# Kernel tuning notes

Measured on AMD Instinct MI355X. Metric: run time of the kernel, lower is better.

## Reference

```python
import jax, jax.numpy as jnp
import numpy as np

EMB = 1280
MD = 200
N = 20000
E = 200000
LN_EPS = 1e-5


def _layer_norm(x, g, b):
    mu = jnp.mean(x, axis=-1, keepdims=True)
    var = jnp.mean((x - mu) ** 2, axis=-1, keepdims=True)
    return (x - mu) * jax.lax.rsqrt(var + LN_EPS) * g + b


def _gat_conv(x, edge_index, edge_attr, W, We, a_src, a_dst, a_edge, bias, heads, C):
    """PyG GATConv (bias-free lin, edge_dim, add_self_loops with fill='mean')."""
    n = x.shape[0]
    src, dst = edge_index[0], edge_index[1]
    # self-loop edge_attr = mean of incoming edge_attr per dst node (0 if none)
    cnt = jax.ops.segment_sum(jnp.ones((edge_attr.shape[0],), x.dtype), dst, n)
    s = jax.ops.segment_sum(edge_attr, dst, n)
    loop_attr = jnp.where(cnt[:, None] > 0, s / jnp.maximum(cnt, 1.0)[:, None], 0.0)
    loop = jnp.arange(n)
    src = jnp.concatenate([src, loop])
    dst = jnp.concatenate([dst, loop])
    ea = jnp.concatenate([edge_attr, loop_attr], axis=0)
    h = (x @ W).reshape(n, heads, C)                      # [N,H,C]
    al_s = jnp.einsum('nhc,hc->nh', h, a_src)
    al_d = jnp.einsum('nhc,hc->nh', h, a_dst)
    eh = (ea @ We).reshape(-1, heads, C)                  # [E+N,H,C]
    al_e = jnp.einsum('ehc,hc->eh', eh, a_edge)
    alpha = jax.nn.leaky_relu(al_s[src] + al_d[dst] + al_e, 0.2)
    amax = jax.ops.segment_max(alpha, dst, n)
    amax = jnp.where(jnp.isfinite(amax), amax, 0.0)
    ex = jnp.exp(alpha - amax[dst])
    denom = jax.ops.segment_sum(ex, dst, n)
    w = ex / (denom[dst] + 1e-16)                         # segment softmax over dst
    out = jax.ops.segment_sum(h[src] * w[:, :, None], dst, n)
    return out.reshape(n, heads * C) + bias


def _forward(x, edge_index, edge_attr,
             ca_qw, ca_qb, ca_kw, ca_kb, ca_vw, ca_vb, ca_ow, ca_ob,
             g0_w, g0_ew, g0_as, g0_ad, g0_ae, g0_b, ln0_g, ln0_b,
             g1_w, g1_ew, g1_as, g1_ad, g1_ae, g1_b, ln1_g, ln1_b,
             g2_w, g2_ew, g2_as, g2_ad, g2_ae, g2_b, ln2_g, ln2_b,
             cls_w1, cls_b1, cls_w2, cls_b2):
    xe = x[:, :EMB]
    md = x[0, EMB:]
    # CrossAttention: single md vector -> K,V are [1,hidden]
    Q = xe @ ca_qw + ca_qb                                # [N,hid]
    K = md @ ca_kw + ca_kb                                # [hid]
    V = md @ ca_vw + ca_vb                                # [hid]
    scores = (Q @ K) / jnp.sqrt(jnp.asarray(Q.shape[-1], Q.dtype))  # [N]
    wts = jax.nn.softmax(scores, axis=0)[:, None]         # softmax over nodes
    attended = wts * V[None, :]                           # [N,hid]
    h = attended @ ca_ow + ca_ob + xe                     # [N,EMB]

    h = _gat_conv(h, edge_index, edge_attr, g0_w, g0_ew, g0_as, g0_ad, g0_ae, g0_b, 4, 256)
    h = jax.nn.relu(_layer_norm(h, ln0_g, ln0_b))
    h = _gat_conv(h, edge_index, edge_attr, g1_w, g1_ew, g1_as, g1_ad, g1_ae, g1_b, 4, 256)
    h = jax.nn.relu(_layer_norm(h, ln1_g, ln1_b))
    h = _gat_conv(h, edge_index, edge_attr, g2_w, g2_ew, g2_as, g2_ad, g2_ae, g2_b, 1, 256)
    h = jax.nn.relu(_layer_norm(h, ln2_g, ln2_b))

    g = jnp.mean(h, axis=0, keepdims=True)                # [1,256]
    g = jax.nn.relu(g @ cls_w1 + cls_b1)
    return g @ cls_w2 + cls_b2                            # [1,2]


def setup_inputs() -> dict:
    key = jax.random.key(0)
    ks = jax.random.split(key, 64)
    i = [0]
    def nrm(shape, scale=0.05):
        i[0] += 1
        return jax.random.normal(ks[i[0]], shape, jnp.float32) * scale
    inp = {}
    inp['x'] = nrm((N, EMB + MD), 1.0)
    inp['edge_index'] = jax.random.randint(ks[60], (2, E), 0, N, jnp.int64 if jax.config.read('jax_enable_x64') else jnp.int32)
    inp['edge_attr'] = jax.random.uniform(ks[61], (E, 1), jnp.float32)
    inp.update(ca_qw=nrm((EMB, 256)), ca_qb=jnp.zeros((256,), jnp.float32),
               ca_kw=nrm((MD, 256)), ca_kb=jnp.zeros((256,), jnp.float32),
               ca_vw=nrm((MD, 256)), ca_vb=jnp.zeros((256,), jnp.float32),
               ca_ow=nrm((256, EMB)), ca_ob=jnp.zeros((EMB,), jnp.float32))
    inp.update(g0_w=nrm((EMB, 1024)), g0_ew=nrm((1, 1024)), g0_as=nrm((4, 256)),
               g0_ad=nrm((4, 256)), g0_ae=nrm((4, 256)), g0_b=jnp.zeros((1024,), jnp.float32),
               ln0_g=jnp.ones((1024,), jnp.float32), ln0_b=jnp.zeros((1024,), jnp.float32))
    inp.update(g1_w=nrm((1024, 1024)), g1_ew=nrm((1, 1024)), g1_as=nrm((4, 256)),
               g1_ad=nrm((4, 256)), g1_ae=nrm((4, 256)), g1_b=jnp.zeros((1024,), jnp.float32),
               ln1_g=jnp.ones((1024,), jnp.float32), ln1_b=jnp.zeros((1024,), jnp.float32))
    inp.update(g2_w=nrm((1024, 256)), g2_ew=nrm((1, 256)), g2_as=nrm((1, 256)),
               g2_ad=nrm((1, 256)), g2_ae=nrm((1, 256)), g2_b=jnp.zeros((256,), jnp.float32),
               ln2_g=jnp.ones((256,), jnp.float32), ln2_b=jnp.zeros((256,), jnp.float32))
    inp.update(cls_w1=nrm((256, 128)), cls_b1=jnp.zeros((128,), jnp.float32),
               cls_w2=nrm((128, 2)), cls_b2=jnp.zeros((2,), jnp.float32))
    return inp


def reference(x, edge_index, edge_attr,
              ca_qw, ca_qb, ca_kw, ca_kb, ca_vw, ca_vb, ca_ow, ca_ob,
              g0_w, g0_ew, g0_as, g0_ad, g0_ae, g0_b, ln0_g, ln0_b,
              g1_w, g1_ew, g1_as, g1_ad, g1_ae, g1_b, ln1_g, ln1_b,
              g2_w, g2_ew, g2_as, g2_ad, g2_ae, g2_b, ln2_g, ln2_b,
              cls_w1, cls_b1, cls_w2, cls_b2):
    return _forward(x, edge_index, edge_attr,
                    ca_qw, ca_qb, ca_kw, ca_kb, ca_vw, ca_vb, ca_ow, ca_ob,
                    g0_w, g0_ew, g0_as, g0_ad, g0_ae, g0_b, ln0_g, ln0_b,
                    g1_w, g1_ew, g1_as, g1_ad, g1_ae, g1_b, ln1_g, ln1_b,
                    g2_w, g2_ew, g2_as, g2_ad, g2_ae, g2_b, ln2_g, ln2_b,
                    cls_w1, cls_b1, cls_w2, cls_b2)
```

## Files before the change

kernel.cpp:

```cpp
#include <hip/hip_runtime.h>
#include <hip/hip_bf16.h>
#include <math.h>

#define N_NODES 20000
#define N_EDGES 200000
#define XROW    1480

typedef __attribute__((ext_vector_type(8))) _Float16 f16x8;
typedef __attribute__((ext_vector_type(8))) unsigned short u16x8;
typedef __attribute__((ext_vector_type(4))) float f32x4v;

__device__ __forceinline__ float wsum(float v){
#pragma unroll
  for (int o=32;o>0;o>>=1) v += __shfl_down(v,o);
  return v;
}
__device__ __forceinline__ float wmax(float v){
#pragma unroll
  for (int o=32;o>0;o>>=1) v = fmaxf(v,__shfl_down(v,o));
  return v;
}
__device__ __forceinline__ float wsum_all(float v){
#pragma unroll
  for (int o=32;o>0;o>>=1) v += __shfl_xor(v,o);
  return v;
}
__device__ __forceinline__ float wmax_all(float v){
#pragma unroll
  for (int o=32;o>0;o>>=1) v = fmaxf(v,__shfl_xor(v,o));
  return v;
}

__device__ __forceinline__ unsigned short f2hu(float f){
  _Float16 h = (_Float16)f;
  return __builtin_bit_cast(unsigned short, h);
}
__device__ __forceinline__ float hu2f(unsigned short u){
  return (float)__builtin_bit_cast(_Float16, u);
}

__device__ __forceinline__ void async_copy16(void* lds, const void* g){
  __builtin_amdgcn_global_load_lds((const __attribute__((address_space(1))) void*)g,
                                   (__attribute__((address_space(3))) void*)lds, 16, 0, 0);
}

__global__ void edge_count_kernel(const int* __restrict__ ei, const float* __restrict__ ea,
                                  int* __restrict__ cnt, float* __restrict__ easum, int E){
  int e = blockIdx.x*256 + threadIdx.x;
  if (e >= E) return;
  int dst = ei[E + e];
  atomicAdd(&cnt[dst], 1);
  atomicAdd(&easum[dst], ea[e]);
}

__launch_bounds__(1024)
__global__ void scan_kernel(const int* __restrict__ cnt, const float* __restrict__ easum,
                            int* __restrict__ off, float* __restrict__ loop_attr, int n){
  __shared__ int buf[1024];
  const int PER = (N_NODES + 1023)/1024;
  int t = threadIdx.x;
  int base = t*PER;
  int local[PER];
  int s = 0;
#pragma unroll
  for (int k=0;k<PER;k++){
    int i = base + k;
    int v = (i<n)? cnt[i] : 0;
    local[k] = v;
    s += v;
  }
  buf[t] = s;
  __syncthreads();
  for (int d2=1; d2<1024; d2<<=1){
    int tv = (t>=d2)? buf[t-d2] : 0;
    __syncthreads();
    buf[t] += tv;
    __syncthreads();
  }
  int run = buf[t] - s;
#pragma unroll
  for (int k=0;k<PER;k++){
    int i = base + k;
    if (i < n){
      off[i] = run;
      int v = local[k];
      loop_attr[i] = (v>0) ? easum[i]/(float)v : 0.f;
      run += v;
    }
  }
  if (t == 1023) off[n] = buf[1023];
}

__global__ void edge_fill_kernel(const int* __restrict__ ei, const float* __restrict__ ea,
                                 const int* __restrict__ off, int* __restrict__ fill,
                                 int* __restrict__ csr_src, float* __restrict__ csr_ea, int E){
  int e = blockIdx.x*256 + threadIdx.x;
  if (e >= E) return;
  int dst = ei[E + e];
  int pos = off[dst] + atomicAdd(&fill[dst], 1);
  csr_src[pos] = ei[e];
  csr_ea[pos]  = ea[e];
}

__global__ void wt_f16_kernel(const float* __restrict__ W, int K, int N,
                              unsigned short* __restrict__ Wt){
  __shared__ float tile[32][33];
  int k0 = blockIdx.x*32, n0 = blockIdx.y*32;
  int tx = threadIdx.x & 31, ty = threadIdx.x >> 5;
  for (int r=ty; r<32; r+=8) tile[r][tx] = W[(size_t)(k0+r)*N + n0+tx];
  __syncthreads();
  for (int r=ty; r<32; r+=8){
    float w = tile[tx][r];
    Wt[(size_t)(n0+r)*K + k0+tx] = f2hu(w);
  }
}

__global__ void kv_kernel(const float* __restrict__ x,
                          const float* __restrict__ kw, const float* __restrict__ kb,
                          const float* __restrict__ vw, const float* __restrict__ vb,
                          float* __restrict__ Kv, float* __restrict__ Vv){
  int j = threadIdx.x;
  float ka = kb[j], va = vb[j];
  for (int k=0;k<200;k++){
    float m = x[1280+k];
    ka = fmaf(m, kw[k*256+j], ka);
    va = fmaf(m, vw[k*256+j], va);
  }
  Kv[j]=ka; Vv[j]=va;
}

__global__ void qkvo_kernel(const float* __restrict__ qw, const float* __restrict__ ow,
                            const float* __restrict__ Kv, const float* __restrict__ Vv,
                            float* __restrict__ qK, float* __restrict__ Vo){
  int b = blockIdx.x;
  if (b < 20){
    int wv = threadIdx.x>>6, lane = threadIdx.x&63;
    float4 k4 = ((const float4*)Kv)[lane];
    int w0 = b*4 + wv;
    for (int r = w0; r < 1280; r += 80){
      float4 q = *(const float4*)(qw + (size_t)r*256 + lane*4);
      float v = q.x*k4.x + q.y*k4.y + q.z*k4.z + q.w*k4.w;
      v = wsum(v);
      if (lane==0) qK[r] = v;
    }
  } else {
    int j = (b-20)*256 + threadIdx.x;
    float a=0;
    for (int i=0;i<256;i++) a = fmaf(Vv[i], ow[(size_t)i*1280+j], a);
    Vo[j]=a;
  }
}

__global__ void obw_kernel(const float* __restrict__ ob, const float* __restrict__ Vo,
                           const float* __restrict__ W, float* __restrict__ obW, float* __restrict__ VoW){
  int j = blockIdx.x*256 + threadIdx.x;
  int i0 = blockIdx.y*128;
  float a=0,b=0;
  for (int i=i0;i<i0+128;i++){
    float w = W[(size_t)i*1024+j];
    a = fmaf(ob[i], w, a);
    b = fmaf(Vo[i], w, b);
  }
  atomicAdd(&obW[j], a);
  atomicAdd(&VoW[j], b);
}

__launch_bounds__(256)
__global__ void xh_scores_kernel(const float* __restrict__ x, const float* __restrict__ qK,
                                 unsigned short* __restrict__ xh, float* __restrict__ scores, int n){
  __shared__ float qs[1280];
  int t = threadIdx.x;
  for (int i=t;i<1280;i+=256) qs[i]=qK[i];
  __syncthreads();
  int wid = t>>6, lane = t&63;
  int node = blockIdx.x*4 + wid;
  if (node >= n) return;
  const float* xr = x + (size_t)node*XROW;
  unsigned short* orow = xh + (size_t)node*1280;
  float acc = 0.f;
#pragma unroll
  for (int it=0; it<5; it++){
    int c4 = it*64 + lane;
    float4 v = *(const float4*)(xr + c4*4);
    ushort4 o;
    o.x = f2hu(v.x); o.y = f2hu(v.y); o.z = f2hu(v.z); o.w = f2hu(v.w);
    *(ushort4*)(orow + c4*4) = o;
    acc = fmaf(v.x, qs[c4*4+0], acc);
    acc = fmaf(v.y, qs[c4*4+1], acc);
    acc = fmaf(v.z, qs[c4*4+2], acc);
    acc = fmaf(v.w, qs[c4*4+3], acc);
  }
  acc = wsum(acc);
  if (lane==0) scores[node] = acc;
}

__launch_bounds__(1024)
__global__ void softmax_nodes(const float* __restrict__ scores, float* __restrict__ wts, int n){
  __shared__ float red[16];
  int t = threadIdx.x, lane=t&63, wid=t>>6;
  float m = -INFINITY;
  for (int i=t;i<n;i+=1024) m = fmaxf(m, scores[i]);
  m = wmax(m);
  if (lane==0) red[wid]=m;
  __syncthreads();
  if (t==0){ float r=red[0]; for (int k=1;k<16;k++) r=fmaxf(r,red[k]); red[0]=r; }
  __syncthreads();
  float M = red[0];
  __syncthreads();
  float z=0;
  for (int i=t;i<n;i+=1024) z += __expf((scores[i]-M)*(1.f/16.f));
  z = wsum(z);
  if (lane==0) red[wid]=z;
  __syncthreads();
  if (t==0){ float r=0; for (int k=0;k<16;k++) r+=red[k]; red[0]=r; }
  __syncthreads();
  float invZ = 1.f/red[0];
  for (int i=t;i<n;i+=1024) wts[i] = __expf((scores[i]-M)*(1.f/16.f))*invZ;
}

__launch_bounds__(256)
__global__ void gemm_f16(const unsigned short* __restrict__ A,
                         const unsigned short* __restrict__ B,
                         unsigned short* __restrict__ C, int M, int N, int K,
                         const float* __restrict__ addCol,
                         const float* __restrict__ vCol,
                         const float* __restrict__ wRow,
                         const float* __restrict__ a_src,
                         const float* __restrict__ a_dst,
                         float* __restrict__ alsp,
                         float* __restrict__ aldp)
{
  __shared__ short lds[2*2*128*32];

  const int ntc = N >> 7;
  const int sh  = __popc(ntc - 1);
  const int g   = blockIdx.y >> sh;
  const int nt  = blockIdx.y & (ntc - 1);
  const int band = blockIdx.x + (g << 3);
  if (band * 128 >= M) return;

  const int t = threadIdx.x;
  const int w = t>>6, l = t&63;
  const int bm = band*128, bn = nt*128;
  const int wr = (w>>1)*64, wc = (w&1)*64;
  const int half = w & 1;

  f32x4v acc[4][4];
#pragma unroll
  for (int i=0;i<4;i++)
#pragma unroll
    for (int j=0;j<4;j++) acc[i][j] = (f32x4v){0.f,0.f,0.f,0.f};

  const unsigned short* Ap[2]; const unsigned short* Bp[2];
  int ldsOff[2];
#pragma unroll
  for (int q=0;q<2;q++){
    int p    = (w*2+q)*64 + l;
    int sr   = p>>3, slot = p&7;
    int sl   = slot ^ (sr&7);
    int r    = sr*2 + (sl>>2);
    int kc   = (sl&3)*8;
    int rowA = bm + r; if (rowA > M-1) rowA = M-1;
    Ap[q] = A + (size_t)rowA*K + kc;
    Bp[q] = B + (size_t)(bn+r)*K + kc;
    ldsOff[q] = (w*2+q)*512;
  }

  const int nsteps = K >> 5;

#pragma unroll
  for (int q=0;q<2;q++) async_copy16(lds + ldsOff[q],        Ap[q]);
#pragma unroll
  for (int q=0;q<2;q++) async_copy16(lds + 4096 + ldsOff[q], Bp[q]);

  const int q4 = l>>4, m16 = l&15;

  for (int kt=0; kt<nsteps; ++kt){
    short* curb = lds + (kt&1)*8192;

    if (kt+1 < nsteps){
      short* nxt = lds + ((kt+1)&1)*8192;
      const int k0n = (kt+1)*32;
#pragma unroll
      for (int q=0;q<2;q++) async_copy16(nxt + ldsOff[q],        Ap[q] + k0n);
#pragma unroll
      for (int q=0;q<2;q++) async_copy16(nxt + 4096 + ldsOff[q], Bp[q] + k0n);
      asm volatile("s_waitcnt vmcnt(4)" ::: "memory");
    } else {
      asm volatile("s_waitcnt vmcnt(0)" ::: "memory");
    }
    __builtin_amdgcn_sched_barrier(0);
    __builtin_amdgcn_s_barrier();
    __builtin_amdgcn_sched_barrier(0);

    __builtin_amdgcn_s_setprio(1);
    {
      f16x8 af[4], bf[4];
#pragma unroll
      for (int i=0;i<4;i++){
        int ra = wr + i*16 + m16;
        af[i] = *(const f16x8*)&curb[(ra>>1)*64 + ((((((ra&1)<<2)+q4)) ^ ((ra>>1)&7))<<3)];
        int rb = wc + i*16 + m16;
        bf[i] = *(const f16x8*)&curb[4096 + (rb>>1)*64 + ((((((rb&1)<<2)+q4)) ^ ((rb>>1)&7))<<3)];
      }
#pragma unroll
      for (int i=0;i<4;i++)
#pragma unroll
        for (int j=0;j<4;j++)
          acc[i][j] = __builtin_amdgcn_mfma_f32_16x16x32_f16(af[i], bf[j], acc[i][j], 0,0,0);
    }
    __builtin_amdgcn_s_setprio(0);
    __builtin_amdgcn_sched_barrier(0);
    __builtin_amdgcn_s_barrier();
    __builtin_amdgcn_sched_barrier(0);
  }

  float* sred = (float*)lds;
  float* dred = sred + 256;
  float asv[4], adv[4];
#pragma unroll
  for (int j=0;j<4;j++){
    int n = bn + wc + j*16 + m16;
    asv[j] = a_src[n];
    adv[j] = a_dst[n];
  }
#pragma unroll
  for (int i=0;i<4;i++){
#pragma unroll
    for (int r=0;r<4;r++){
      int rloc = wr + i*16 + q4*4 + r;
      int m = bm + rloc;
      float wrow = addCol ? wRow[m < M ? m : M-1] : 0.f;
      float vj[4];
#pragma unroll
      for (int j=0;j<4;j++){
        int n = bn + wc + j*16 + m16;
        float v = acc[i][j][r];
        if (addCol) v += addCol[n] + wrow*vCol[n];
        vj[j] = v;
      }
      if (m < M){
        unsigned short* crow = C + (size_t)m*N;
#pragma unroll
        for (int j=0;j<4;j++) crow[bn + wc + j*16 + m16] = f2hu(vj[j]);
      }
      float s = vj[0]*asv[0] + vj[1]*asv[1] + vj[2]*asv[2] + vj[3]*asv[3];
      float d = vj[0]*adv[0] + vj[1]*adv[1] + vj[2]*adv[2] + vj[3]*adv[3];
#pragma unroll
      for (int o=1;o<16;o<<=1){ s += __shfl_xor(s,o); d += __shfl_xor(d,o); }
      if (m16 == 0){
        sred[half*128 + rloc] = s;
        dred[half*128 + rloc] = d;
      }
    }
  }
  __syncthreads();
  if (t < 128){
    int m = bm + t;
    if (m < M){
      alsp[(size_t)nt*M + m] = sred[t] + sred[128+t];
      aldp[(size_t)nt*M + m] = dred[t] + dred[128+t];
    }
  }
}

__global__ void als_combine(const float* __restrict__ alsp, const float* __restrict__ aldp,
                            float* __restrict__ als, float* __restrict__ ald, int M, int H,
                            const float* __restrict__ We, const float* __restrict__ a_edge,
                            float* __restrict__ we){
  if (blockIdx.x == 0){
    int wid = threadIdx.x>>6, lane = threadIdx.x&63;
    if (wid < H){
      const float4* w4 = (const float4*)(We + wid*256);
      const float4* a4 = (const float4*)(a_edge + wid*256);
      float4 a = w4[lane], b = a4[lane];
      float v = a.x*b.x + a.y*b.y + a.z*b.z + a.w*b.w;
      v = wsum(v);
      if (lane==0) we[wid]=v;
    }
  }
  int idx = blockIdx.x*256 + threadIdx.x;
  if (idx >= M*H) return;
  int m = idx / H, hh = idx - m*H;
  als[idx] = alsp[(size_t)(2*hh)*M + m] + alsp[(size_t)(2*hh+1)*M + m];
  ald[idx] = aldp[(size_t)(2*hh)*M + m] + aldp[(size_t)(2*hh+1)*M + m];
}

template<int H>
__launch_bounds__(256)
__global__ void gat_agg_ln_wave(const unsigned short* __restrict__ hmat,
                           const float* __restrict__ als, const float* __restrict__ ald,
                           const int* __restrict__ off, const int* __restrict__ csr_src,
                           const float* __restrict__ csr_ea, const float* __restrict__ loop_attr,
                           const float* __restrict__ we,
                           const float* __restrict__ bias,
                           const float* __restrict__ ln_g, const float* __restrict__ ln_b,
                           float* __restrict__ outf, unsigned short* __restrict__ outb, int n)
{
  constexpr int OUT = 256*H;
  constexpr int CPL = OUT/64;
  const int wv = threadIdx.x>>6, lane = threadIdx.x&63;
  const int i = blockIdx.x*4 + wv;
  __shared__ float wbuf_s[4][64*H];
  __shared__ int   sbuf_s[4][64];
  if (i >= n) return;
  float* wbuf = wbuf_s[wv];
  int*   sbuf = sbuf_s[wv];

  const int begin = off[i];
  const int deg   = off[i+1]-begin;
  const int S     = deg + 1;

  float aldi[H], wei[H];
#pragma unroll
  for (int hh=0;hh<H;hh++){ aldi[hh]=ald[(size_t)i*H+hh]; wei[hh]=we[hh]; }
  const float lea = loop_attr[i];

  const int head = (lane*CPL) >> 8;
  const int c0   = lane*CPL;
  float acc[CPL];
#pragma unroll
  for (int c=0;c<CPL;c++) acc[c]=0.f;

  if (S <= 64){
    int src = i; float ev = lea;
    if (lane < deg){ src = csr_src[begin+lane]; ev = csr_ea[begin+lane]; }
    const bool act = lane < S;
    sbuf[lane] = src;

    if constexpr (CPL==16){
      u16x8 a0r0,a0r1,a1r0,a1r1;
      {
        const unsigned short* r0p = hmat + (size_t)sbuf[0]*OUT + c0;
        a0r0 = *(const u16x8*)r0p; a0r1 = *(const u16x8*)(r0p+8);
        a1r0 = a0r0; a1r1 = a0r1;
        if (S > 1){
          const unsigned short* r1p = hmat + (size_t)sbuf[1]*OUT + c0;
          a1r0 = *(const u16x8*)r1p; a1r1 = *(const u16x8*)(r1p+8);
        }
      }
      float a[H];
#pragma unroll
      for (int hh=0;hh<H;hh++){
        float v = als[(size_t)src*H+hh] + aldi[hh] + ev*wei[hh];
        a[hh] = v>0.f ? v : 0.2f*v;
      }
#pragma unroll
      for (int hh=0;hh<H;hh++){
        float M = wmax_all(act ? a[hh] : -INFINITY);
        float e = act ? __expf(a[hh]-M) : 0.f;
        float Z = wsum_all(e);
        wbuf[lane*H+hh] = e / (Z + 1e-16f);
      }
      int j = 0;
      for (; j+2<S; j+=2){
        u16x8 n0r0,n0r1,n1r0,n1r1;
        {
          const unsigned short* rp = hmat + (size_t)sbuf[j+2]*OUT + c0;
          n0r0 = *(const u16x8*)rp; n0r1 = *(const u16x8*)(rp+8);
          n1r0 = n0r0; n1r1 = n0r1;
          if (j+3 < S){
            const unsigned short* rq = hmat + (size_t)sbuf[j+3]*OUT + c0;
            n1r0 = *(const u16x8*)rq; n1r1 = *(const u16x8*)(rq+8);
          }
        }
        float w0 = wbuf[j*H+head], w1 = wbuf[(j+1)*H+head];
#pragma unroll
        for (int c=0;c<8;c++){
          acc[c]   = fmaf(w0, hu2f(a0r0[c]), acc[c]);
          acc[8+c] = fmaf(w0, hu2f(a0r1[c]), acc[8+c]);
        }
#pragma unroll
        for (int c=0;c<8;c++){
          acc[c]   = fmaf(w1, hu2f(a1r0[c]), acc[c]);
          acc[8+c] = fmaf(w1, hu2f(a1r1[c]), acc[8+c]);
        }
        a0r0=n0r0; a0r1=n0r1; a1r0=n1r0; a1r1=n1r1;
      }
      {
        float w0 = wbuf[j*H+head];
#pragma unroll
        for (int c=0;c<8;c++){
          acc[c]   = fmaf(w0, hu2f(a0r0[c]), acc[c]);
          acc[8+c] = fmaf(w0, hu2f(a0r1[c]), acc[8+c]);
        }
        if (j+1 < S){
          float w1 = wbuf[(j+1)*H+head];
#pragma unroll
          for (int c=0;c<8;c++){
            acc[c]   = fmaf(w1, hu2f(a1r0[c]), acc[c]);
            acc[8+c] = fmaf(w1, hu2f(a1r1[c]), acc[8+c]);
          }
        }
      }
    } else {
      ushort4 a0, a1;
      {
        a0 = *(const ushort4*)(hmat + (size_t)sbuf[0]*OUT + c0);
        a1 = a0;
        if (S > 1) a1 = *(const ushort4*)(hmat + (size_t)sbuf[1]*OUT + c0);
      }
      float a[H];
#pragma unroll
      for (int hh=0;hh<H;hh++){
        float v = als[(size_t)src*H+hh] + aldi[hh] + ev*wei[hh];
        a[hh] = v>0.f ? v : 0.2f*v;
      }
#pragma unroll
      for (int hh=0;hh<H;hh++){
        float M = wmax_all(act ? a[hh] : -INFINITY);
        float e = act ? __expf(a[hh]-M) : 0.f;
        float Z = wsum_all(e);
        wbuf[lane*H+hh] = e / (Z + 1e-16f);
      }
      int j = 0;
      for (; j+2<S; j+=2){
        ushort4 n0, n1;
        n0 = *(const ushort4*)(hmat + (size_t)sbuf[j+2]*OUT + c0);
        n1 = n0;
        if (j+3 < S) n1 = *(const ushort4*)(hmat + (size_t)sbuf[j+3]*OUT + c0);
        float w0 = wbuf[j*H+head], w1 = wbuf[(j+1)*H+head];
        acc[0]=fmaf(w0,hu2f(a0.x),acc[0]); acc[1]=fmaf(w0,hu2f(a0.y),acc[1]);
        acc[2]=fmaf(w0,hu2f(a0.z),acc[2]); acc[3]=fmaf(w0,hu2f(a0.w),acc[3]);
        acc[0]=fmaf(w1,hu2f(a1.x),acc[0]); acc[1]=fmaf(w1,hu2f(a1.y),acc[1]);
        acc[2]=fmaf(w1,hu2f(a1.z),acc[2]); acc[3]=fmaf(w1,hu2f(a1.w),acc[3]);
        a0=n0; a1=n1;
      }
      {
        float w0 = wbuf[j*H+head];
        acc[0]=fmaf(w0,hu2f(a0.x),acc[0]); acc[1]=fmaf(w0,hu2f(a0.y),acc[1]);
        acc[2]=fmaf(w0,hu2f(a0.z),acc[2]); acc[3]=fmaf(w0,hu2f(a0.w),acc[3]);
        if (j+1 < S){
          float w1 = wbuf[(j+1)*H+head];
          acc[0]=fmaf(w1,hu2f(a1.x),acc[0]); acc[1]=fmaf(w1,hu2f(a1.y),acc[1]);
          acc[2]=fmaf(w1,hu2f(a1.z),acc[2]); acc[3]=fmaf(w1,hu2f(a1.w),acc[3]);
        }
      }
    }
  } else {
    float rm[H];
#pragma unroll
    for (int hh=0;hh<H;hh++) rm[hh] = -INFINITY;
    for (int s=lane; s<S; s+=64){
      int src = (s<deg)? csr_src[begin+s] : i;
      float ev = (s<deg)? csr_ea[begin+s] : lea;
#pragma unroll
      for (int hh=0;hh<H;hh++){
        float v = als[(size_t)src*H+hh] + aldi[hh] + ev*wei[hh];
        v = v>0.f? v : 0.2f*v;
        rm[hh] = fmaxf(rm[hh], v);
      }
    }
    float M[H], es[H];
#pragma unroll
    for (int hh=0;hh<H;hh++){ M[hh]=wmax_all(rm[hh]); es[hh]=0.f; }
    for (int s=lane; s<S; s+=64){
      int src = (s<deg)? csr_src[begin+s] : i;
      float ev = (s<deg)? csr_ea[begin+s] : lea;
#pragma unroll
      for (int hh=0;hh<H;hh++){
        float v = als[(size_t)src*H+hh] + aldi[hh] + ev*wei[hh];
        v = v>0.f? v : 0.2f*v;
        es[hh] += __expf(v - M[hh]);
      }
    }
    float invZ[H];
#pragma unroll
    for (int hh=0;hh<H;hh++) invZ[hh] = 1.f/(wsum_all(es[hh]) + 1e-16f);
    for (int cb=0; cb<S; cb+=64){
      int m = min(64, S-cb);
      int s = cb + lane;
      if (s < S){
        int src = (s<deg)? csr_src[begin+s] : i;
        float ev = (s<deg)? csr_ea[begin+s] : lea;
        sbuf[lane] = src;
#pragma unroll
        for (int hh=0;hh<H;hh++){
          float v = als[(size_t)src*H+hh] + aldi[hh] + ev*wei[hh];
          v = v>0.f? v : 0.2f*v;
          wbuf[lane*H+hh] = __expf(v - M[hh]) * invZ[hh];
        }
      }
      for (int j=0;j<m;j++){
        int sj = sbuf[j];
        float wj = wbuf[j*H+head];
        const unsigned short* row = hmat + (size_t)sj*OUT + c0;
        if constexpr (CPL==16){
          u16x8 r0 = *(const u16x8*)(row);
          u16x8 r1 = *(const u16x8*)(row+8);
#pragma unroll
          for (int c=0;c<8;c++){
            acc[c]   = fmaf(wj, hu2f(r0[c]), acc[c]);
            acc[8+c] = fmaf(wj, hu2f(r1[c]), acc[8+c]);
          }
        } else {
          ushort4 r = *(const ushort4*)(row);
          acc[0]=fmaf(wj,hu2f(r.x),acc[0]); acc[1]=fmaf(wj,hu2f(r.y),acc[1]);
          acc[2]=fmaf(wj,hu2f(r.z),acc[2]); acc[3]=fmaf(wj,hu2f(r.w),acc[3]);
        }
      }
    }
  }

  float vals[CPL];
  float ls=0.f;
#pragma unroll
  for (int c=0;c<CPL;c+=4){
    float4 b4 = *(const float4*)(bias + c0 + c);
    vals[c]=acc[c]+b4.x; vals[c+1]=acc[c+1]+b4.y; vals[c+2]=acc[c+2]+b4.z; vals[c+3]=acc[c+3]+b4.w;
    ls += vals[c]+vals[c+1]+vals[c+2]+vals[c+3];
  }
  float mu = wsum_all(ls) * (1.f/OUT);
  float lv=0.f;
#pragma unroll
  for (int c=0;c<CPL;c++){ float d=vals[c]-mu; lv += d*d; }
  float inv = rsqrtf(wsum_all(lv)*(1.f/OUT) + 1e-5f);

  if (outb){
    if constexpr (CPL==16){
#pragma unroll
      for (int c=0;c<CPL;c+=8){
        u16x8 o;
#pragma unroll
        for (int k=0;k<8;k++){
          float g = ln_g[c0+c+k], b = ln_b[c0+c+k];
          o[k] = f2hu(fmaxf((vals[c+k]-mu)*inv*g + b, 0.f));
        }
        *(u16x8*)(outb + (size_t)i*OUT + c0 + c) = o;
      }
    } else {
      ushort4 o;
      o.x = f2hu(fmaxf((vals[0]-mu)*inv*ln_g[c0+0] + ln_b[c0+0], 0.f));
      o.y = f2hu(fmaxf((vals[1]-mu)*inv*ln_g[c0+1] + ln_b[c0+1], 0.f));
      o.z = f2hu(fmaxf((vals[2]-mu)*inv*ln_g[c0+2] + ln_b[c0+2], 0.f));
      o.w = f2hu(fmaxf((vals[3]-mu)*inv*ln_g[c0+3] + ln_b[c0+3], 0.f));
      *(ushort4*)(outb + (size_t)i*OUT + c0) = o;
    }
  } else {
#pragma unroll
    for (int c=0;c<CPL;c+=4){
      float4 g4 = *(const float4*)(ln_g + c0 + c);
      float4 b4 = *(const float4*)(ln_b + c0 + c);
      float4 o;
      o.x = fmaxf((vals[c+0]-mu)*inv*g4.x + b4.x, 0.f);
      o.y = fmaxf((vals[c+1]-mu)*inv*g4.y + b4.y, 0.f);
      o.z = fmaxf((vals[c+2]-mu)*inv*g4.z + b4.z, 0.f);
      o.w = fmaxf((vals[c+3]-mu)*inv*g4.w + b4.w, 0.f);
      *(float4*)(outf + (size_t)i*OUT + c0 + c) = o;
    }
  }
}

__global__ void colsum_kernel(const float* __restrict__ h2, float* __restrict__ gsum, int n){
  int c = threadIdx.x;
  float acc=0;
  for (int i=blockIdx.x;i<n;i+=gridDim.x) acc += h2[(size_t)i*256 + c];
  atomicAdd(&gsum[c], acc);
}

__launch_bounds__(128)
__global__ void cls_kernel(const float* __restrict__ gsum,
                           const float* __restrict__ w1, const float* __restrict__ b1,
                           const float* __restrict__ w2, const float* __restrict__ b2,
                           float* __restrict__ outp){
  __shared__ float g[256];
  __shared__ float hid[128];
  int t = threadIdx.x;
  g[t]     = gsum[t]    *(1.f/N_NODES);
  g[t+128] = gsum[t+128]*(1.f/N_NODES);
  __syncthreads();
  float a = b1[t];
  for (int c=0;c<256;c++) a = fmaf(g[c], w1[c*128+t], a);
  hid[t] = fmaxf(a, 0.f);
  __syncthreads();
  if (t<2){
    float o = b2[t];
    for (int j=0;j<128;j++) o = fmaf(hid[j], w2[j*2+t], o);
    outp[t] = o;
  }
}

extern "C" void kernel_launch(void* const* d_in, const int* in_sizes, int n_in,
                              void* d_out, int out_size, void* d_ws, size_t ws_size,
                              hipStream_t stream)
{
  const float* x      = (const float*)d_in[0];
  const int*   ei     = (const int*)  d_in[1];
  const float* ea     = (const float*)d_in[2];
  const float* ca_qw  = (const float*)d_in[3];
  const float* ca_kw  = (const float*)d_in[5];
  const float* ca_kb  = (const float*)d_in[6];
  const float* ca_vw  = (const float*)d_in[7];
  const float* ca_vb  = (const float*)d_in[8];
  const float* ca_ow  = (const float*)d_in[9];
  const float* ca_ob  = (const float*)d_in[10];
  const float* g0_w   = (const float*)d_in[11];
  const float* g0_ew  = (const float*)d_in[12];
  const float* g0_as  = (const float*)d_in[13];
  const float* g0_ad  = (const float*)d_in[14];
  const float* g0_ae  = (const float*)d_in[15];
  const float* g0_b   = (const float*)d_in[16];
  const float* ln0_g  = (const float*)d_in[17];
  const float* ln0_b  = (const float*)d_in[18];
  const float* g1_w   = (const float*)d_in[19];
  const float* g1_ew  = (const float*)d_in[20];
  const float* g1_as  = (const float*)d_in[21];
  const float* g1_ad  = (const float*)d_in[22];
  const float* g1_ae  = (const float*)d_in[23];
  const float* g1_b   = (const float*)d_in[24];
  const float* ln1_g  = (const float*)d_in[25];
  const float* ln1_b  = (const float*)d_in[26];
  const float* g2_w   = (const float*)d_in[27];
  const float* g2_ew  = (const float*)d_in[28];
  const float* g2_as  = (const float*)d_in[29];
  const float* g2_ad  = (const float*)d_in[30];
  const float* g2_ae  = (const float*)d_in[31];
  const float* g2_b   = (const float*)d_in[32];
  const float* ln2_g  = (const float*)d_in[33];
  const float* ln2_b  = (const float*)d_in[34];
  const float* cls_w1 = (const float*)d_in[35];
  const float* cls_b1 = (const float*)d_in[36];
  const float* cls_w2 = (const float*)d_in[37];
  const float* cls_b2 = (const float*)d_in[38];
  float* outp = (float*)d_out;

  const int N = N_NODES, E = N_EDGES;

  char* base = (char*)d_ws;
  size_t o = 0;
  auto alloc = [&](size_t bytes)->void*{
    void* p = base + o;
    o += (bytes + 255) & ~(size_t)255;
    return p;
  };
  unsigned short* hF   = (unsigned short*)alloc((size_t)N*1024*2);
  unsigned short* Af   = (unsigned short*)alloc((size_t)N*1280*2);
  float*          h2   = (float*)         alloc((size_t)N*256*4);
  unsigned short* Wt   = (unsigned short*)alloc((size_t)1280*1024*2);
  float* alsp      = (float*)alloc((size_t)8*N*4);
  float* aldp      = (float*)alloc((size_t)8*N*4);
  float* als       = (float*)alloc((size_t)2*N*4*4);
  float* ald       = als + (size_t)N*4;
  float* scores    = (float*)alloc((size_t)N*4);
  float* wts       = (float*)alloc((size_t)N*4);
  int*   cnt       = (int*)  alloc((size_t)N*4);
  float* easum     = (float*)alloc((size_t)N*4);
  int*   off       = (int*)  alloc((size_t)(N+1)*4);
  int*   fill      = (int*)  alloc((size_t)N*4);
  int*   csr_src   = (int*)  alloc((size_t)E*4);
  float* csr_ea    = (float*)alloc((size_t)E*4);
  float* loop_attr = (float*)alloc((size_t)N*4);
  float* Kv        = (float*)alloc(256*4);
  float* Vv        = (float*)alloc(256*4);
  float* qK        = (float*)alloc(1280*4);
  float* Vo        = (float*)alloc(1280*4);
  float* obW       = (float*)alloc(1024*4);
  float* VoW       = (float*)alloc(1024*4);
  float* web       = (float*)alloc(16*4);
  float* gsum      = (float*)alloc(256*4);

  hipMemsetAsync(cnt,   0, (size_t)N*4, stream);
  hipMemsetAsync(easum, 0, (size_t)N*4, stream);
  hipMemsetAsync(fill,  0, (size_t)N*4, stream);
  hipMemsetAsync(gsum,  0, 256*4,       stream);
  hipMemsetAsync(obW,   0, 1024*4,      stream);
  hipMemsetAsync(VoW,   0, 1024*4,      stream);

  int eblocks = (E + 255)/256;
  edge_count_kernel<<<eblocks,256,0,stream>>>(ei, ea, cnt, easum, E);
  scan_kernel<<<1,1024,0,stream>>>(cnt, easum, off, loop_attr, N);
  edge_fill_kernel<<<eblocks,256,0,stream>>>(ei, ea, off, fill, csr_src, csr_ea, E);

  kv_kernel<<<1,256,0,stream>>>(x, ca_kw, ca_kb, ca_vw, ca_vb, Kv, Vv);
  qkvo_kernel<<<25,256,0,stream>>>(ca_qw, ca_ow, Kv, Vv, qK, Vo);
  xh_scores_kernel<<<(N+3)/4,256,0,stream>>>(x, qK, Af, scores, N);
  obw_kernel<<<dim3(4,10),256,0,stream>>>(ca_ob, Vo, g0_w, obW, VoW);
  softmax_nodes<<<1,1024,0,stream>>>(scores, wts, N);

  const int mTiles  = (N + 127)/128;
  const int mGroups = (mTiles + 7)/8;
  const int NB4 = (N + 3)/4;

  wt_f16_kernel<<<dim3(1280/32, 1024/32),256,0,stream>>>(g0_w, 1280, 1024, Wt);
  gemm_f16<<<dim3(8, mGroups*8),256,0,stream>>>(Af, Wt, hF, N, 1024, 1280, obW, VoW, wts,
                                                g0_as, g0_ad, alsp, aldp);
  als_combine<<<(N*4+255)/256,256,0,stream>>>(alsp, aldp, als, ald, N, 4, g0_ew, g0_ae, web);
  gat_agg_ln_wave<4><<<NB4,256,0,stream>>>(hF, als, ald, off, csr_src, csr_ea, loop_attr,
                                           web, g0_b, ln0_g, ln0_b, nullptr, Af, N);

  wt_f16_kernel<<<dim3(1024/32, 1024/32),256,0,stream>>>(g1_w, 1024, 1024, Wt);
  gemm_f16<<<dim3(8, mGroups*8),256,0,stream>>>(Af, Wt, hF, N, 1024, 1024, nullptr, nullptr, nullptr,
                                                g1_as, g1_ad, alsp, aldp);
  als_combine<<<(N*4+255)/256,256,0,stream>>>(alsp, aldp, als, ald, N, 4, g1_ew, g1_ae, web);
  gat_agg_ln_wave<4><<<NB4,256,0,stream>>>(hF, als, ald, off, csr_src, csr_ea, loop_attr,
                                           web, g1_b, ln1_g, ln1_b, nullptr, Af, N);

  wt_f16_kernel<<<dim3(1024/32, 256/32),256,0,stream>>>(g2_w, 1024, 256, Wt);
  gemm_f16<<<dim3(8, mGroups*2),256,0,stream>>>(Af, Wt, hF, N, 256, 1024, nullptr, nullptr, nullptr,
                                                g2_as, g2_ad, alsp, aldp);
  als_combine<<<(N+255)/256,256,0,stream>>>(alsp, aldp, als, ald, N, 1, g2_ew, g2_ae, web);
  gat_agg_ln_wave<1><<<NB4,256,0,stream>>>(hF, als, ald, off, csr_src, csr_ea, loop_attr,
                                           web, g2_b, ln2_g, ln2_b, h2, nullptr, N);

  colsum_kernel<<<256,256,0,stream>>>(h2, gsum, N);
  cls_kernel<<<1,128,0,stream>>>(gsum, cls_w1, cls_b1, cls_w2, cls_b2, outp);

  (void)in_sizes; (void)n_in; (void)out_size; (void)ws_size;
}
```

Measured before the change: 798.8 us.

## Parallelize node softmax and KV projection across blocks, fold normalization into GEMM

Replaces the single-block node softmax with multi-block max and sum-of-exp kernels that combine results through global atomics, using an order-preserving integer encoding for the float max. The per-row softmax weight is now computed inside the first GEMM epilogue from the raw score, the global max and the sum, so the weights array is no longer written. The K/V projection is split across 8 blocks with atomic accumulation. This removes serial single-block kernels from the critical path, at the cost of extra memsets, an extra launch, and nondeterministic float atomic summation.

```diff
diff --git a/kernel.cpp b/kernel.cpp
--- a/kernel.cpp
+++ b/kernel.cpp
@@ -37,6 +37,15 @@
 }
 __device__ __forceinline__ float hu2f(unsigned short u){
   return (float)__builtin_bit_cast(_Float16, u);
+}
+
+__device__ __forceinline__ unsigned fenc(float f){
+  unsigned b = __float_as_uint(f);
+  return (b & 0x80000000u) ? ~b : (b | 0x80000000u);
+}
+__device__ __forceinline__ float fdec(unsigned u){
+  unsigned b = (u & 0x80000000u) ? (u & 0x7FFFFFFFu) : ~u;
+  return __uint_as_float(b);
 }
 
 __device__ __forceinline__ void async_copy16(void* lds, const void* g){
@@ -120,13 +129,16 @@
                           const float* __restrict__ vw, const float* __restrict__ vb,
                           float* __restrict__ Kv, float* __restrict__ Vv){
   int j = threadIdx.x;
-  float ka = kb[j], va = vb[j];
-  for (int k=0;k<200;k++){
+  int k0 = blockIdx.x*25;
+  float ka = 0.f, va = 0.f;
+  if (blockIdx.x == 0){ ka = kb[j]; va = vb[j]; }
+  for (int k=k0;k<k0+25;k++){
     float m = x[1280+k];
     ka = fmaf(m, kw[k*256+j], ka);
     va = fmaf(m, vw[k*256+j], va);
   }
-  Kv[j]=ka; Vv[j]=va;
+  atomicAdd(&Kv[j], ka);
+  atomicAdd(&Vv[j], va);
 }
 
 __global__ void qkvo_kernel(const float* __restrict__ qw, const float* __restrict__ ow,
@@ -194,28 +206,32 @@
   if (lane==0) scores[node] = acc;
 }
 
-__launch_bounds__(1024)
-__global__ void softmax_nodes(const float* __restrict__ scores, float* __restrict__ wts, int n){
-  __shared__ float red[16];
-  int t = threadIdx.x, lane=t&63, wid=t>>6;
+__global__ void smax_kernel(const float* __restrict__ scores, unsigned* __restrict__ gmaxu, int n){
+  __shared__ float red[4];
+  int t = threadIdx.x, lane = t&63, wv = t>>6;
   float m = -INFINITY;
-  for (int i=t;i<n;i+=1024) m = fmaxf(m, scores[i]);
-  m = wmax(m);
-  if (lane==0) red[wid]=m;
+  for (int i = blockIdx.x*256 + t; i < n; i += gridDim.x*256) m = fmaxf(m, scores[i]);
+  m = wmax_all(m);
+  if (lane==0) red[wv] = m;
   __syncthreads();
-  if (t==0){ float r=red[0]; for (int k=1;k<16;k++) r=fmaxf(r,red[k]); red[0]=r; }
+  if (t==0){
+    float r = fmaxf(fmaxf(red[0],red[1]), fmaxf(red[2],red[3]));
+    atomicMax(gmaxu, fenc(r));
+  }
+}
+
+__global__ void zsum_kernel(const float* __restrict__ scores, const unsigned* __restrict__ gmaxu,
+                            float* __restrict__ gz, int n){
+  __shared__ float red[4];
+  float M = fdec(*gmaxu);
+  int t = threadIdx.x, lane = t&63, wv = t>>6;
+  float z = 0.f;
+  for (int i = blockIdx.x*256 + t; i < n; i += gridDim.x*256)
+    z += __expf((scores[i]-M)*(1.f/16.f));
+  z = wsum_all(z);
+  if (lane==0) red[wv] = z;
   __syncthreads();
-  float M = red[0];
-  __syncthreads();
-  float z=0;
-  for (int i=t;i<n;i+=1024) z += __expf((scores[i]-M)*(1.f/16.f));
-  z = wsum(z);
-  if (lane==0) red[wid]=z;
-  __syncthreads();
-  if (t==0){ float r=0; for (int k=0;k<16;k++) r+=red[k]; red[0]=r; }
-  __syncthreads();
-  float invZ = 1.f/red[0];
-  for (int i=t;i<n;i+=1024) wts[i] = __expf((scores[i]-M)*(1.f/16.f))*invZ;
+  if (t==0) atomicAdd(gz, red[0]+red[1]+red[2]+red[3]);
 }
 
 __launch_bounds__(256)
@@ -224,7 +240,9 @@
                          unsigned short* __restrict__ C, int M, int N, int K,
                          const float* __restrict__ addCol,
                          const float* __restrict__ vCol,
-                         const float* __restrict__ wRow,
+                         const float* __restrict__ scoresRow,
+                         const unsigned* __restrict__ gmaxu,
+                         const float* __restrict__ gz,
                          const float* __restrict__ a_src,
                          const float* __restrict__ a_dst,
                          float* __restrict__ alsp,
@@ -315,6 +333,8 @@
     __builtin_amdgcn_sched_barrier(0);
   }
 
+  float Msc = 0.f, invZ = 0.f;
+  if (addCol){ Msc = fdec(*gmaxu); invZ = 1.f/(*gz); }
   float* sred = (float*)lds;
   float* dred = sred + 256;
   float asv[4], adv[4];
@@ -330,7 +350,7 @@
     for (int r=0;r<4;r++){
       int rloc = wr + i*16 + q4*4 + r;
       int m = bm + rloc;
-      float wrow = addCol ? wRow[m < M ? m : M-1] : 0.f;
+      float wrow = addCol ? __expf((scoresRow[m < M ? m : M-1]-Msc)*(1.f/16.f))*invZ : 0.f;
       float vj[4];
 #pragma unroll
       for (int j=0;j<4;j++){
@@ -758,6 +778,9 @@
   float* VoW       = (float*)alloc(1024*4);
   float* web       = (float*)alloc(16*4);
   float* gsum      = (float*)alloc(256*4);
+  unsigned* gmaxu  = (unsigned*)alloc(4);
+  float*    gz     = (float*)alloc(4);
+  (void)wts;
 
   hipMemsetAsync(cnt,   0, (size_t)N*4, stream);
   hipMemsetAsync(easum, 0, (size_t)N*4, stream);
@@ -765,38 +788,46 @@
   hipMemsetAsync(gsum,  0, 256*4,       stream);
   hipMemsetAsync(obW,   0, 1024*4,      stream);
   hipMemsetAsync(VoW,   0, 1024*4,      stream);
+  hipMemsetAsync(Kv,    0, 256*4,       stream);
+  hipMemsetAsync(Vv,    0, 256*4,       stream);
+  hipMemsetAsync(gmaxu, 0, 4,           stream);
+  hipMemsetAsync(gz,    0, 4,           stream);
 
   int eblocks = (E + 255)/256;
   edge_count_kernel<<<eblocks,256,0,stream>>>(ei, ea, cnt, easum, E);
   scan_kernel<<<1,1024,0,stream>>>(cnt, easum, off, loop_attr, N);
   edge_fill_kernel<<<eblocks,256,0,stream>>>(ei, ea, off, fill, csr_src, csr_ea, E);
 
-  kv_kernel<<<1,256,0,stream>>>(x, ca_kw, ca_kb, ca_vw, ca_vb, Kv, Vv);
+  kv_kernel<<<8,256,0,stream>>>(x, ca_kw, ca_kb, ca_vw, ca_vb, Kv, Vv);
   qkvo_kernel<<<25,256,0,stream>>>(ca_qw, ca_ow, Kv, Vv, qK, Vo);
   xh_scores_kernel<<<(N+3)/4,256,0,stream>>>(x, qK, Af, scores, N);
+  smax_kernel<<<40,256,0,stream>>>(scores, gmaxu, N);
+  zsum_kernel<<<40,256,0,stream>>>(scores, gmaxu, gz, N);
   obw_kernel<<<dim3(4,10),256,0,stream>>>(ca_ob, Vo, g0_w, obW, VoW);
-  softmax_nodes<<<1,1024,0,stream>>>(scores, wts, N);
 
   const int mTiles  = (N + 127)/128;
   const int mGroups = (mTiles + 7)/8;
   const int NB4 = (N + 3)/4;
 
   wt_f16_kernel<<<dim3(1280/32, 1024/32),256,0,stream>>>(g0_w, 1280, 1024, Wt);
-  gemm_f16<<<dim3(8, mGroups*8),256,0,stream>>>(Af, Wt, hF, N, 1024, 1280, obW, VoW, wts,
+  gemm_f16<<<dim3(8, mGroups*8),256,0,stream>>>(Af, Wt, hF, N, 1024, 1280, obW, VoW,
+                                                scores, gmaxu, gz,
                                                 g0_as, g0_ad, alsp, aldp);
   als_combine<<<(N*4+255)/256,256,0,stream>>>(alsp, aldp, als, ald, N, 4, g0_ew, g0_ae, web);
   gat_agg_ln_wave<4><<<NB4,256,0,stream>>>(hF, als, ald, off, csr_src, csr_ea, loop_attr,
                                            web, g0_b, ln0_g, ln0_b, nullptr, Af, N);
 
   wt_f16_kernel<<<dim3(1024/32, 1024/32),256,0,stream>>>(g1_w, 1024, 1024, Wt);
-  gemm_f16<<<dim3(8, mGroups*8),256,0,stream>>>(Af, Wt, hF, N, 1024, 1024, nullptr, nullptr, nullptr,
+  gemm_f16<<<dim3(8, mGroups*8),256,0,stream>>>(Af, Wt, hF, N, 1024, 1024, nullptr, nullptr,
+                                                nullptr, nullptr, nullptr,
                                                 g1_as, g1_ad, alsp, aldp);
   als_combine<<<(N*4+255)/256,256,0,stream>>>(alsp, aldp, als, ald, N, 4, g1_ew, g1_ae, web);
   gat_agg_ln_wave<4><<<NB4,256,0,stream>>>(hF, als, ald, off, csr_src, csr_ea, loop_attr,
                                            web, g1_b, ln1_g, ln1_b, nullptr, Af, N);
 
   wt_f16_kernel<<<dim3(1024/32, 256/32),256,0,stream>>>(g2_w, 1024, 256, Wt);
-  gemm_f16<<<dim3(8, mGroups*2),256,0,stream>>>(Af, Wt, hF, N, 256, 1024, nullptr, nullptr, nullptr,
+  gemm_f16<<<dim3(8, mGroups*2),256,0,stream>>>(Af, Wt, hF, N, 256, 1024, nullptr, nullptr,
+                                                nullptr, nullptr, nullptr,
                                                 g2_as, g2_ad, alsp, aldp);
   als_combine<<<(N+255)/256,256,0,stream>>>(alsp, aldp, als, ald, N, 1, g2_ew, g2_ae, web);
   gat_agg_ln_wave<1><<<NB4,256,0,stream>>>(hF, als, ald, off, csr_src, csr_ea, loop_attr,
```

New measurement: 800.4 us. Within noise of the previous version (+0.2%).
